# Kernel optimization log

Hardware: AMD Instinct MI355X
Metric: run time of the kernel (lower is better)

## Reference

```python
import jax, jax.numpy as jnp
import numpy as np


def _unfold(x, k, pad, stride):
    # torch F.unfold: [B,C,H,W] -> [B, C*k*k, L] with (C, kh, kw) channel-major ordering
    B, C, H, W = x.shape
    xp = jnp.pad(x, ((0, 0), (0, 0), (pad, pad), (pad, pad)))
    oh = (H + 2 * pad - k) // stride + 1
    ow = (W + 2 * pad - k) // stride + 1
    rows = (jnp.arange(oh) * stride)[:, None] + jnp.arange(k)[None, :]  # [oh,k]
    cols = (jnp.arange(ow) * stride)[:, None] + jnp.arange(k)[None, :]  # [ow,k]
    p = xp[:, :, rows][:, :, :, :, cols]          # [B,C,oh,k,ow,k]
    p = p.transpose(0, 1, 3, 5, 2, 4)             # [B,C,k,k,oh,ow]
    return p.reshape(B, C * k * k, oh * ow)


def _fold(p, out_hw, k, pad, stride):
    # torch F.fold: overlap-add of patches [B, C*k*k, L] -> [B,C,H,W]
    B = p.shape[0]
    C = p.shape[1] // (k * k)
    H, W = out_hw
    oh = (H + 2 * pad - k) // stride + 1
    ow = (W + 2 * pad - k) // stride + 1
    p = p.reshape(B, C, k, k, oh, ow).transpose(0, 1, 4, 2, 5, 3)  # [B,C,oh,k,ow,k]
    rows = (jnp.arange(oh) * stride)[:, None] + jnp.arange(k)[None, :]  # [oh,k]
    cols = (jnp.arange(ow) * stride)[:, None] + jnp.arange(k)[None, :]  # [ow,k]
    out = jnp.zeros((B, C, H + 2 * pad, W + 2 * pad), p.dtype)
    out = out.at[:, :, rows[:, :, None, None], cols[None, None, :, :]].add(p)
    return out[:, :, pad:pad + H, pad:pad + W]


def _bis_gather(unf, idx):
    # torch.gather along dim=2 with per-batch index broadcast over channels
    return jnp.take_along_axis(unf, idx[:, None, :], axis=2)


def setup_inputs() -> dict:
    key = jax.random.key(0)
    k1, k2, k3, k4 = jax.random.split(key, 4)
    B, H, W = 4, 96, 96
    L = H * W
    return {
        "R_lv2_star_arg": jax.random.randint(k1, (B, L), 0, L, dtype=jnp.int64 if jax.config.jax_enable_x64 else jnp.int32).astype(jnp.int32),
        "lrsr_lv2": jax.random.normal(k2, (B, 64, H, W), dtype=jnp.float32),
        "ref_lv1": jax.random.normal(k3, (B, 64, 2 * H, 2 * W), dtype=jnp.float32),
        "ref_lv2": jax.random.normal(k4, (B, 128, H, W), dtype=jnp.float32),
    }


def reference(R_lv2_star_arg, lrsr_lv2, ref_lv1, ref_lv2):
    H, W = lrsr_lv2.shape[2], lrsr_lv2.shape[3]
    ref_lv2_unfold = _unfold(ref_lv2, 3, 1, 1)   # [B, C2*9, H*W]
    ref_lv1_unfold = _unfold(ref_lv1, 6, 2, 2)   # [B, C1*36, H*W]
    T_lv2_unfold = _bis_gather(ref_lv2_unfold, R_lv2_star_arg)
    T_lv1_unfold = _bis_gather(ref_lv1_unfold, R_lv2_star_arg)
    T_lv2 = _fold(T_lv2_unfold, (H, W), 3, 1, 1) / 9.0
    T_lv1 = _fold(T_lv1_unfold, (2 * H, 2 * W), 6, 2, 2) / 9.0
    return (T_lv2, T_lv1)
```

## Files before the change

### kernel.cpp

```cpp
#include <hip/hip_runtime.h>


typedef float f2 __attribute__((ext_vector_type(2)));
typedef float f4 __attribute__((ext_vector_type(4)));

#define NINE_INV (1.0f / 9.0f)
#define ZCELL 9216u

__device__ __forceinline__ unsigned rne_bf16(float f) {
    unsigned u = __builtin_bit_cast(unsigned, f);
    return (u + 0x7fffu + ((u >> 16) & 1u)) >> 16;
}
__device__ __forceinline__ unsigned pack_bf2(float a, float b) {
    return rne_bf16(a) | (rne_bf16(b) << 16);
}
__device__ __forceinline__ f2 up2(unsigned w) {
    f2 r;
    r.x = __builtin_bit_cast(float, w << 16);
    r.y = __builtin_bit_cast(float, w & 0xffff0000u);
    return r;
}
template <typename T> __device__ __forceinline__ T ntload(const T* p) {
    return __builtin_nontemporal_load(p);
}
template <typename T> __device__ __forceinline__ void ntstore(T* p, T v) {
    __builtin_nontemporal_store(v, p);
}

__global__ __launch_bounds__(256) void table_kernel(
    const int* __restrict__ idx, uint4* __restrict__ tabA,
    unsigned short* __restrict__ tabB)
{
    int g = blockIdx.x * 256 + threadIdx.x;
    int b = g / 9216;
    int u = g - b * 9216;
    const int* idxb = idx + b * 9216;
    int r = u / 96, t = u - 96 * r;
    unsigned e[9];
#pragma unroll
    for (int i = 0; i < 3; ++i) {
        int oy = r - 1 + i;
        bool oyv = (unsigned)oy < 96u;
#pragma unroll
        for (int j = 0; j < 3; ++j) {
            int ox = t - 1 + j;
            bool pv = oyv & ((unsigned)ox < 96u);
            int jv = idxb[pv ? oy * 96 + ox : 0];
            int jy = jv / 96, jx = jv - 96 * jy;
            int ysh = jy + 1 - i, xsh = jx + 1 - j;
            bool sv = pv & ((unsigned)ysh < 96u) & ((unsigned)xsh < 96u);
            e[i * 3 + j] = sv ? (unsigned)(ysh * 96 + xsh) : ZCELL;
        }
    }
    uint4 w;
    w.x = e[0] | (e[1] << 16);
    w.y = e[2] | (e[3] << 16);
    w.z = e[4] | (e[5] << 16);
    w.w = e[6] | (e[7] << 16);
    tabA[g] = w;
    tabB[g] = (unsigned short)e[8];
}

template <bool TAB>
__global__ __launch_bounds__(512, 4) void transfer_kernel(
    const int* __restrict__ idx,
    const float* __restrict__ ref1,
    const float* __restrict__ ref2,
    const uint4* __restrict__ tabA,
    const unsigned short* __restrict__ tabB,
    float* __restrict__ out)
{
    __shared__ __align__(16) unsigned s2[18436];
    const int tid = threadIdx.x;
    const int bid = blockIdx.x;
    const int b = bid & 3;

    if (tid < 4) s2[18432 + tid] = 0;

    const uint4* tA = tabA + b * 9216;
    const unsigned short* tB = tabB + b * 9216;
    const int* idxb = idx + b * 9216;

    auto inline_cells = [&](int u, unsigned* e) {
        int r = u / 96, t = u - 96 * r;
#pragma unroll
        for (int i = 0; i < 3; ++i) {
            int oy = r - 1 + i;
            bool oyv = (unsigned)oy < 96u;
#pragma unroll
            for (int j = 0; j < 3; ++j) {
                int ox = t - 1 + j;
                bool pv = oyv & ((unsigned)ox < 96u);
                int jv = idxb[pv ? oy * 96 + ox : 0];
                int jy = jv / 96, jx = jv - 96 * jy;
                int ysh = jy + 1 - i, xsh = jx + 1 - j;
                bool sv = pv & ((unsigned)ysh < 96u) & ((unsigned)xsh < 96u);
                e[i * 3 + j] = sv ? (unsigned)(ysh * 96 + xsh) : ZCELL;
            }
        }
    };

    auto do_taps = [&](const unsigned* cw, unsigned c8, f2& a0, f2& a1) {
#pragma unroll
        for (int q = 0; q < 4; ++q) {
            unsigned lo = cw[q] & 0xffffu, hi = cw[q] >> 16;
            uint2 wa = *(const uint2*)((const char*)s2 + (lo << 3));
            uint2 wb = *(const uint2*)((const char*)s2 + (hi << 3));
            a0 += up2(wa.x); a1 += up2(wa.y);
            a0 += up2(wb.x); a1 += up2(wb.y);
        }
        uint2 wc = *(const uint2*)((const char*)s2 + (c8 << 3));
        a0 += up2(wc.x); a1 += up2(wc.y);
    };

    if (bid < 256) {
        const int q = (bid >> 2) & 1, c0 = (bid >> 3) * 2;
        const float* g0 = ref1 + (size_t)(b * 64 + c0) * 36864;

        for (int u2 = tid; u2 < 4608; u2 += 512) {
            int ysh = u2 / 48, xsh0 = 2 * (u2 - 48 * ysh);
            const float* gp = g0 + (size_t)(2 * ysh + q) * 192 + 2 * xsh0;
            f4 va = ntload((const f4*)gp);
            f4 vb = ntload((const f4*)(gp + 36864));
            uint4 w;
            w.x = pack_bf2(va.x, va.y); w.y = pack_bf2(vb.x, vb.y);
            w.z = pack_bf2(va.z, va.w); w.w = pack_bf2(vb.z, vb.w);
            *(uint4*)(s2 + 4 * u2) = w;
        }
        __syncthreads();

        float* ob = out + 4718592 + (size_t)(b * 64 + c0) * 36864;

        uint4 cA; unsigned cB;
        if (TAB) { cA = tA[tid]; cB = tB[tid]; }
        int u = tid;
#pragma unroll 2
        for (int k = 0; k < 18; ++k) {
            uint4 nA = cA; unsigned nB = cB;
            if (TAB && k < 17) { nA = tA[u + 512]; nB = tB[u + 512]; }
            unsigned cw[4];
            unsigned c8;
            if (TAB) {
                cw[0] = cA.x; cw[1] = cA.y; cw[2] = cA.z; cw[3] = cA.w; c8 = cB;
            } else {
                unsigned e[9];
                inline_cells(u, e);
                cw[0] = e[0] | (e[1] << 16); cw[1] = e[2] | (e[3] << 16);
                cw[2] = e[4] | (e[5] << 16); cw[3] = e[6] | (e[7] << 16);
                c8 = e[8];
            }
            f2 a0 = {0.f, 0.f}, a1 = {0.f, 0.f};
            do_taps(cw, c8, a0, a1);
            f2 nv = {NINE_INV, NINE_INV};
            a0 *= nv; a1 *= nv;
            int r = u / 96, t = u - 96 * r;
            float* op = ob + (size_t)(2 * r + q) * 192 + 2 * t;
            ntstore((f2*)op, a0);
            ntstore((f2*)(op + 36864), a1);
            u += 512; cA = nA; cB = nB;
        }
    } else {
        const int r2 = bid - 256;
        const int grp = (r2 >> 2) & 31, h = (r2 >> 7) & 1;
        const int c0 = grp * 4;
        const float* g0 = ref2 + (size_t)(b * 128 + c0) * 9216;

        for (int u2 = tid; u2 < 4608; u2 += 512) {
            f2 p0 = ntload((const f2*)(g0 + 2 * u2));
            f2 p1 = ntload((const f2*)(g0 + 9216 + 2 * u2));
            f2 p2 = ntload((const f2*)(g0 + 2 * 9216 + 2 * u2));
            f2 p3 = ntload((const f2*)(g0 + 3 * 9216 + 2 * u2));
            uint4 w;
            w.x = pack_bf2(p0.x, p1.x); w.y = pack_bf2(p2.x, p3.x);
            w.z = pack_bf2(p0.y, p1.y); w.w = pack_bf2(p2.y, p3.y);
            *(uint4*)(s2 + 4 * u2) = w;
        }
        __syncthreads();

        float* ob = out + (size_t)(b * 128 + c0) * 9216;

        const int u0 = h * 4608;
        uint4 cA; unsigned cB;
        if (TAB) { cA = tA[u0 + tid]; cB = tB[u0 + tid]; }
        int u = u0 + tid;
#pragma unroll 2
        for (int k = 0; k < 9; ++k) {
            uint4 nA = cA; unsigned nB = cB;
            if (TAB && k < 8) { nA = tA[u + 512]; nB = tB[u + 512]; }
            unsigned cw[4];
            unsigned c8;
            if (TAB) {
                cw[0] = cA.x; cw[1] = cA.y; cw[2] = cA.z; cw[3] = cA.w; c8 = cB;
            } else {
                unsigned e[9];
                inline_cells(u, e);
                cw[0] = e[0] | (e[1] << 16); cw[1] = e[2] | (e[3] << 16);
                cw[2] = e[4] | (e[5] << 16); cw[3] = e[6] | (e[7] << 16);
                c8 = e[8];
            }
            f2 a0 = {0.f, 0.f}, a1 = {0.f, 0.f};
            do_taps(cw, c8, a0, a1);
            f2 nv = {NINE_INV, NINE_INV};
            a0 *= nv; a1 *= nv;
            float* op = ob + u;
            ntstore(op, a0.x);          ntstore(op + 9216, a0.y);
            ntstore(op + 2 * 9216, a1.x); ntstore(op + 3 * 9216, a1.y);
            u += 512; cA = nA; cB = nB;
        }
    }
}

extern "C" void kernel_launch(void* const* d_in, const int* in_sizes, int n_in,
                              void* d_out, int out_size, void* d_ws, size_t ws_size,
                              hipStream_t stream) {
    const int*   idx  = (const int*)d_in[0];
    const float* ref1 = (const float*)d_in[2];
    const float* ref2 = (const float*)d_in[3];
    float* outp = (float*)d_out;

    uint4* tabA = (uint4*)d_ws;
    unsigned short* tabB = (unsigned short*)((char*)d_ws + (size_t)4 * 9216 * 16);

    const size_t need = (size_t)4 * 9216 * 16 + (size_t)4 * 9216 * 2;
    if (ws_size >= need) {
        hipLaunchKernelGGL(table_kernel, dim3(144), dim3(256), 0, stream,
                           idx, tabA, tabB);
        hipLaunchKernelGGL(transfer_kernel<true>, dim3(512), dim3(512), 0, stream,
                           idx, ref1, ref2, tabA, tabB, outp);
    } else {
        hipLaunchKernelGGL(transfer_kernel<false>, dim3(512), dim3(512), 0, stream,
                           idx, ref1, ref2, tabA, tabB, outp);
    }
}
```

Baseline: 28.06 us.

## Fuse table build into transfer kernel via cooperative grid sync

Merges the separate table-building kernel into the main transfer kernel, launched cooperatively. Each block builds a slice of the index table and stages its channel data into LDS, then a grid-wide sync makes the table visible before the gather-and-fold phase. This removes one kernel launch and its launch gap, and overlaps table construction with the shared-memory staging loads. In exchange it adds a grid barrier and requires all 512 blocks to be co-resident, which is allowed by the 4-blocks-per-CU launch bounds but may still fail or serialize.

```diff
diff --git a/kernel.cpp b/kernel.cpp
--- a/kernel.cpp
+++ b/kernel.cpp
@@ -1,5 +1,8 @@
 #include <hip/hip_runtime.h>
-
+#include <hip/hip_cooperative_groups.h>
+
+
+namespace cg = cooperative_groups;
 
 typedef float f2 __attribute__((ext_vector_type(2)));
 typedef float f4 __attribute__((ext_vector_type(4)));
@@ -27,11 +30,10 @@
     __builtin_nontemporal_store(v, p);
 }
 
-__global__ __launch_bounds__(256) void table_kernel(
-    const int* __restrict__ idx, uint4* __restrict__ tabA,
-    unsigned short* __restrict__ tabB)
+__device__ __forceinline__ void build_entry(const int* __restrict__ idx, int g,
+                                            uint4* __restrict__ tabA,
+                                            unsigned short* __restrict__ tabB)
 {
-    int g = blockIdx.x * 256 + threadIdx.x;
     int b = g / 9216;
     int u = g - b * 9216;
     const int* idxb = idx + b * 9216;
@@ -61,13 +63,12 @@
     tabB[g] = (unsigned short)e[8];
 }
 
-template <bool TAB>
-__global__ __launch_bounds__(512, 4) void transfer_kernel(
+__global__ __launch_bounds__(512, 4) void transfer_coop(
     const int* __restrict__ idx,
     const float* __restrict__ ref1,
     const float* __restrict__ ref2,
-    const uint4* __restrict__ tabA,
-    const unsigned short* __restrict__ tabB,
+    uint4* __restrict__ tabA,
+    unsigned short* __restrict__ tabB,
     float* __restrict__ out)
 {
     __shared__ __align__(16) unsigned s2[18436];
@@ -77,9 +78,122 @@
 
     if (tid < 4) s2[18432 + tid] = 0;
 
+    {
+        int g = bid * 512 + tid;
+        if (g < 36864) build_entry(idx, g, tabA, tabB);
+    }
+
     const uint4* tA = tabA + b * 9216;
     const unsigned short* tB = tabB + b * 9216;
+    const f2 nv = {NINE_INV, NINE_INV};
+
+    auto do_taps = [&](const unsigned* cw, unsigned c8, f2& a0, f2& a1) {
+#pragma unroll
+        for (int q = 0; q < 4; ++q) {
+            unsigned lo = cw[q] & 0xffffu, hi = cw[q] >> 16;
+            uint2 wa = *(const uint2*)((const char*)s2 + (lo << 3));
+            uint2 wb = *(const uint2*)((const char*)s2 + (hi << 3));
+            a0 += up2(wa.x); a1 += up2(wa.y);
+            a0 += up2(wb.x); a1 += up2(wb.y);
+        }
+        uint2 wc = *(const uint2*)((const char*)s2 + (c8 << 3));
+        a0 += up2(wc.x); a1 += up2(wc.y);
+    };
+
+    if (bid < 256) {
+        const int q = (bid >> 2) & 1, c0 = (bid >> 3) * 2;
+        const float* g0 = ref1 + (size_t)(b * 64 + c0) * 36864;
+
+        for (int u2 = tid; u2 < 4608; u2 += 512) {
+            int ysh = u2 / 48, xsh0 = 2 * (u2 - 48 * ysh);
+            const float* gp = g0 + (size_t)(2 * ysh + q) * 192 + 2 * xsh0;
+            f4 va = ntload((const f4*)gp);
+            f4 vb = ntload((const f4*)(gp + 36864));
+            uint4 w;
+            w.x = pack_bf2(va.x, va.y); w.y = pack_bf2(vb.x, vb.y);
+            w.z = pack_bf2(va.z, va.w); w.w = pack_bf2(vb.z, vb.w);
+            *(uint4*)(s2 + 4 * u2) = w;
+        }
+
+        cg::this_grid().sync();
+
+        float* ob = out + 4718592 + (size_t)(b * 64 + c0) * 36864;
+
+        uint4 cA = tA[tid]; unsigned cB = tB[tid];
+        int u = tid;
+#pragma unroll 2
+        for (int k = 0; k < 18; ++k) {
+            uint4 nA = cA; unsigned nB = cB;
+            if (k < 17) { nA = tA[u + 512]; nB = tB[u + 512]; }
+            unsigned cw[4];
+            cw[0] = cA.x; cw[1] = cA.y; cw[2] = cA.z; cw[3] = cA.w;
+            unsigned c8 = cB;
+            f2 a0 = {0.f, 0.f}, a1 = {0.f, 0.f};
+            do_taps(cw, c8, a0, a1);
+            a0 *= nv; a1 *= nv;
+            int r = u / 96, t = u - 96 * r;
+            float* op = ob + (size_t)(2 * r + q) * 192 + 2 * t;
+            ntstore((f2*)op, a0);
+            ntstore((f2*)(op + 36864), a1);
+            u += 512; cA = nA; cB = nB;
+        }
+    } else {
+        const int r2 = bid - 256;
+        const int grp = (r2 >> 2) & 31, h = (r2 >> 7) & 1;
+        const int c0 = grp * 4;
+        const float* g0 = ref2 + (size_t)(b * 128 + c0) * 9216;
+
+        for (int u2 = tid; u2 < 4608; u2 += 512) {
+            f2 p0 = ntload((const f2*)(g0 + 2 * u2));
+            f2 p1 = ntload((const f2*)(g0 + 9216 + 2 * u2));
+            f2 p2 = ntload((const f2*)(g0 + 2 * 9216 + 2 * u2));
+            f2 p3 = ntload((const f2*)(g0 + 3 * 9216 + 2 * u2));
+            uint4 w;
+            w.x = pack_bf2(p0.x, p1.x); w.y = pack_bf2(p2.x, p3.x);
+            w.z = pack_bf2(p0.y, p1.y); w.w = pack_bf2(p2.y, p3.y);
+            *(uint4*)(s2 + 4 * u2) = w;
+        }
+
+        cg::this_grid().sync();
+
+        float* ob = out + (size_t)(b * 128 + c0) * 9216;
+
+        const int u0 = h * 4608;
+        uint4 cA = tA[u0 + tid]; unsigned cB = tB[u0 + tid];
+        int u = u0 + tid;
+#pragma unroll 2
+        for (int k = 0; k < 9; ++k) {
+            uint4 nA = cA; unsigned nB = cB;
+            if (k < 8) { nA = tA[u + 512]; nB = tB[u + 512]; }
+            unsigned cw[4];
+            cw[0] = cA.x; cw[1] = cA.y; cw[2] = cA.z; cw[3] = cA.w;
+            unsigned c8 = cB;
+            f2 a0 = {0.f, 0.f}, a1 = {0.f, 0.f};
+            do_taps(cw, c8, a0, a1);
+            a0 *= nv; a1 *= nv;
+            float* op = ob + u;
+            ntstore(op, a0.x);            ntstore(op + 9216, a0.y);
+            ntstore(op + 2 * 9216, a1.x); ntstore(op + 3 * 9216, a1.y);
+            u += 512; cA = nA; cB = nB;
+        }
+    }
+}
+
+__global__ __launch_bounds__(512, 4) void transfer_fallback(
+    const int* __restrict__ idx,
+    const float* __restrict__ ref1,
+    const float* __restrict__ ref2,
+    float* __restrict__ out)
+{
+    __shared__ __align__(16) unsigned s2[18436];
+    const int tid = threadIdx.x;
+    const int bid = blockIdx.x;
+    const int b = bid & 3;
+
+    if (tid < 4) s2[18432 + tid] = 0;
+
     const int* idxb = idx + b * 9216;
+    const f2 nv = {NINE_INV, NINE_INV};
 
     auto inline_cells = [&](int u, unsigned* e) {
         int r = u / 96, t = u - 96 * r;
@@ -99,24 +213,17 @@
             }
         }
     };
-
-    auto do_taps = [&](const unsigned* cw, unsigned c8, f2& a0, f2& a1) {
-#pragma unroll
-        for (int q = 0; q < 4; ++q) {
-            unsigned lo = cw[q] & 0xffffu, hi = cw[q] >> 16;
-            uint2 wa = *(const uint2*)((const char*)s2 + (lo << 3));
-            uint2 wb = *(const uint2*)((const char*)s2 + (hi << 3));
-            a0 += up2(wa.x); a1 += up2(wa.y);
-            a0 += up2(wb.x); a1 += up2(wb.y);
-        }
-        uint2 wc = *(const uint2*)((const char*)s2 + (c8 << 3));
-        a0 += up2(wc.x); a1 += up2(wc.y);
+    auto do_taps9 = [&](const unsigned* e, f2& a0, f2& a1) {
+#pragma unroll
+        for (int p = 0; p < 9; ++p) {
+            uint2 w = *(const uint2*)((const char*)s2 + (e[p] << 3));
+            a0 += up2(w.x); a1 += up2(w.y);
+        }
     };
 
     if (bid < 256) {
         const int q = (bid >> 2) & 1, c0 = (bid >> 3) * 2;
         const float* g0 = ref1 + (size_t)(b * 64 + c0) * 36864;
-
         for (int u2 = tid; u2 < 4608; u2 += 512) {
             int ysh = u2 / 48, xsh0 = 2 * (u2 - 48 * ysh);
             const float* gp = g0 + (size_t)(2 * ysh + q) * 192 + 2 * xsh0;
@@ -128,43 +235,23 @@
             *(uint4*)(s2 + 4 * u2) = w;
         }
         __syncthreads();
-
         float* ob = out + 4718592 + (size_t)(b * 64 + c0) * 36864;
-
-        uint4 cA; unsigned cB;
-        if (TAB) { cA = tA[tid]; cB = tB[tid]; }
-        int u = tid;
-#pragma unroll 2
-        for (int k = 0; k < 18; ++k) {
-            uint4 nA = cA; unsigned nB = cB;
-            if (TAB && k < 17) { nA = tA[u + 512]; nB = tB[u + 512]; }
-            unsigned cw[4];
-            unsigned c8;
-            if (TAB) {
-                cw[0] = cA.x; cw[1] = cA.y; cw[2] = cA.z; cw[3] = cA.w; c8 = cB;
-            } else {
-                unsigned e[9];
-                inline_cells(u, e);
-                cw[0] = e[0] | (e[1] << 16); cw[1] = e[2] | (e[3] << 16);
-                cw[2] = e[4] | (e[5] << 16); cw[3] = e[6] | (e[7] << 16);
-                c8 = e[8];
-            }
+        for (int u = tid; u < 9216; u += 512) {
+            unsigned e[9];
+            inline_cells(u, e);
             f2 a0 = {0.f, 0.f}, a1 = {0.f, 0.f};
-            do_taps(cw, c8, a0, a1);
-            f2 nv = {NINE_INV, NINE_INV};
+            do_taps9(e, a0, a1);
             a0 *= nv; a1 *= nv;
             int r = u / 96, t = u - 96 * r;
             float* op = ob + (size_t)(2 * r + q) * 192 + 2 * t;
             ntstore((f2*)op, a0);
             ntstore((f2*)(op + 36864), a1);
-            u += 512; cA = nA; cB = nB;
         }
     } else {
         const int r2 = bid - 256;
         const int grp = (r2 >> 2) & 31, h = (r2 >> 7) & 1;
         const int c0 = grp * 4;
         const float* g0 = ref2 + (size_t)(b * 128 + c0) * 9216;
-
         for (int u2 = tid; u2 < 4608; u2 += 512) {
             f2 p0 = ntload((const f2*)(g0 + 2 * u2));
             f2 p1 = ntload((const f2*)(g0 + 9216 + 2 * u2));
@@ -176,36 +263,17 @@
             *(uint4*)(s2 + 4 * u2) = w;
         }
         __syncthreads();
-
         float* ob = out + (size_t)(b * 128 + c0) * 9216;
-
         const int u0 = h * 4608;
-        uint4 cA; unsigned cB;
-        if (TAB) { cA = tA[u0 + tid]; cB = tB[u0 + tid]; }
-        int u = u0 + tid;
-#pragma unroll 2
-        for (int k = 0; k < 9; ++k) {
-            uint4 nA = cA; unsigned nB = cB;
-            if (TAB && k < 8) { nA = tA[u + 512]; nB = tB[u + 512]; }
-            unsigned cw[4];
-            unsigned c8;
-            if (TAB) {
-                cw[0] = cA.x; cw[1] = cA.y; cw[2] = cA.z; cw[3] = cA.w; c8 = cB;
-            } else {
-                unsigned e[9];
-                inline_cells(u, e);
-                cw[0] = e[0] | (e[1] << 16); cw[1] = e[2] | (e[3] << 16);
-                cw[2] = e[4] | (e[5] << 16); cw[3] = e[6] | (e[7] << 16);
-                c8 = e[8];
-            }
+        for (int u = u0 + tid; u < u0 + 4608; u += 512) {
+            unsigned e[9];
+            inline_cells(u, e);
             f2 a0 = {0.f, 0.f}, a1 = {0.f, 0.f};
-            do_taps(cw, c8, a0, a1);
-            f2 nv = {NINE_INV, NINE_INV};
+            do_taps9(e, a0, a1);
             a0 *= nv; a1 *= nv;
             float* op = ob + u;
-            ntstore(op, a0.x);          ntstore(op + 9216, a0.y);
+            ntstore(op, a0.x);            ntstore(op + 9216, a0.y);
             ntstore(op + 2 * 9216, a1.x); ntstore(op + 3 * 9216, a1.y);
-            u += 512; cA = nA; cB = nB;
         }
     }
 }
@@ -223,12 +291,12 @@
 
     const size_t need = (size_t)4 * 9216 * 16 + (size_t)4 * 9216 * 2;
     if (ws_size >= need) {
-        hipLaunchKernelGGL(table_kernel, dim3(144), dim3(256), 0, stream,
-                           idx, tabA, tabB);
-        hipLaunchKernelGGL(transfer_kernel<true>, dim3(512), dim3(512), 0, stream,
-                           idx, ref1, ref2, tabA, tabB, outp);
+        void* args[] = {(void*)&idx, (void*)&ref1, (void*)&ref2,
+                        (void*)&tabA, (void*)&tabB, (void*)&outp};
+        hipLaunchCooperativeKernel((const void*)transfer_coop,
+                                   dim3(512), dim3(512), args, 0, stream);
     } else {
-        hipLaunchKernelGGL(transfer_kernel<false>, dim3(512), dim3(512), 0, stream,
-                           idx, ref1, ref2, tabA, tabB, outp);
-    }
-}
+        hipLaunchKernelGGL(transfer_fallback, dim3(512), dim3(512), 0, stream,
+                           idx, ref1, ref2, outp);
+    }
+}
```

Measured after the change: 91.80 us. +227.2%, slower.
